# Kernel optimization log

Hardware: AMD Instinct MI355X
Metric: run time of the kernel (lower is better)

## Reference

```python
import jax, jax.numpy as jnp
import numpy as np

GROUP_SIZE = 64
M, K, N, RANK = 4096, 4096, 4096, 32


def setup_inputs() -> dict:
    key = jax.random.key(0)
    ks = jax.random.split(key, 7)
    x = jax.random.normal(ks[0], (M, K), dtype=jnp.float32)
    # int4 weight residual in [-8, 7]
    q_w = jax.random.randint(ks[1], (K, N), -8, 8, dtype=jnp.int32)
    # positive per-group weight scales, shape (K // group_size, N)
    wscales = jax.random.uniform(ks[2], (K // GROUP_SIZE, N), dtype=jnp.float32) * 0.01 + 1e-4
    lora_down = jax.random.normal(ks[3], (K, RANK), dtype=jnp.float32) * 0.02
    lora_up = jax.random.normal(ks[4], (RANK, N), dtype=jnp.float32) * 0.02
    # smoothing factors, strictly positive
    smooth = jax.random.uniform(ks[5], (K,), dtype=jnp.float32) + 0.5
    bias = jax.random.normal(ks[6], (N,), dtype=jnp.float32)
    return {"x": x, "q_w": q_w, "wscales": wscales, "lora_down": lora_down,
            "lora_up": lora_up, "smooth": smooth, "bias": bias}


def reference(x, q_w, wscales, lora_down, lora_up, smooth, bias):
    G = GROUP_SIZE
    m, k = x.shape
    n = q_w.shape[1]
    ng = k // G  # groups along K

    # smooth activation: move outliers into weights
    x_smooth = x / smooth[None, :]

    # per-group symmetric int4 quantize + dequantize of activations
    xg = x_smooth.reshape(m, ng, G)
    ascales = jnp.maximum(jnp.max(jnp.abs(xg), axis=-1) / 7.0, 1e-8)  # (m, ng)
    qx = jnp.clip(jnp.round(xg / ascales[..., None]), -8.0, 7.0)
    x_dq = (qx * ascales[..., None]).reshape(m, k)

    # dequantize int4 weight residual: grouped along K
    W_dq = (q_w.astype(jnp.float32).reshape(ng, G, n) * wscales[:, None, :]).reshape(k, n)

    # simulated int4 GEMM + fp LoRA residual + bias
    y_main = x_dq @ W_dq
    y_lora = (x @ lora_down) @ lora_up
    return y_main + y_lora + bias[None, :]
```

## Files before the change

kernel.cpp:

```cpp
#include <hip/hip_runtime.h>
#include <hip/hip_bf16.h>
#include <stdint.h>

#define GSIZE 64
#define MDIM 4096
#define KDIM 4096
#define NDIM 4096
#define RANK 32
#define KE   4160
#define NG   64
#define NSPLIT 8

#define N_LORATQ 256
#define N_WPREP  (65 * 64)
#define NBLOCKS  (N_LORATQ + N_WPREP)

typedef __bf16 bf16x4 __attribute__((ext_vector_type(4)));
typedef __bf16 bf16x8 __attribute__((ext_vector_type(8)));
typedef float  f32x4  __attribute__((ext_vector_type(4)));

#define GPTR(p) ((__attribute__((address_space(1))) void*)(uintptr_t)(p))
#define LPTR(p) ((__attribute__((address_space(3))) void*)(p))

__global__ __launch_bounds__(512) void k_prep(const float* __restrict__ x,
                                              const int*   __restrict__ qw,
                                              const float* __restrict__ wsc,
                                              const float* __restrict__ ld,
                                              const float* __restrict__ lu,
                                              const float* __restrict__ smooth,
                                              __bf16* __restrict__ A,
                                              __bf16* __restrict__ Wt,
                                              float* __restrict__ tws) {
    __shared__ __attribute__((aligned(16))) char smem[81920];
    int b   = blockIdx.x;
    int tid = threadIdx.x;

    if (b < N_LORATQ) {
        __bf16* Xs  = (__bf16*)smem;
        __bf16* BsL = (__bf16*)(smem + 65536);
        int m0 = (b & 31) * 128;
        int sp = b >> 5;
        int lane = tid & 63;
        int wave = tid >> 6;
        int quad = lane >> 4;
        int mrow = lane & 15;
        int c4   = tid & 63;

        f32x4 z = {0.f, 0.f, 0.f, 0.f};
        f32x4 acc[2];
        acc[0] = z; acc[1] = z;

        #pragma unroll
        for (int sub = 0; sub < 2; ++sub) {
            int kb = sp * 512 + sub * 256;

            #pragma unroll
            for (int i = 0; i < 16; ++i) {
                int idx = i * 512 + tid;
                int k = idx >> 5, n = idx & 31;
                *(__bf16*)((char*)BsL + n * 512 +
                           ((((k >> 3) ^ (n & 7)) << 4) | ((k & 7) << 1)))
                    = (__bf16)ld[(size_t)(kb + k) * RANK + n];
            }

            {
                float4 sv = *(const float4*)(smooth + kb + c4 * 4);
                float4 si = {__builtin_amdgcn_rcpf(sv.x), __builtin_amdgcn_rcpf(sv.y),
                             __builtin_amdgcn_rcpf(sv.z), __builtin_amdgcn_rcpf(sv.w)};
                int g = c4 >> 1;
                #pragma unroll 4
                for (int p = 0; p < 16; ++p) {
                    int row = wave + 8 * p;
                    float4 xv = *(const float4*)(x + (size_t)(m0 + row) * KDIM + kb + c4 * 4);
                    float4 xs = {xv.x * si.x, xv.y * si.y, xv.z * si.z, xv.w * si.w};
                    float a = fmaxf(fmaxf(fabsf(xs.x), fabsf(xs.y)),
                                    fmaxf(fabsf(xs.z), fabsf(xs.w)));
                    #pragma unroll
                    for (int off = 1; off < 16; off <<= 1)
                        a = fmaxf(a, __shfl_xor(a, off, 64));
                    float ascale = fmaxf(a * (1.0f / 7.0f), 1e-8f);
                    float rin = __builtin_amdgcn_rcpf(ascale);
                    float q0 = fminf(fmaxf(rintf(xs.x * rin), -8.f), 7.f);
                    float q1 = fminf(fmaxf(rintf(xs.y * rin), -8.f), 7.f);
                    float q2 = fminf(fmaxf(rintf(xs.z * rin), -8.f), 7.f);
                    float q3 = fminf(fmaxf(rintf(xs.w * rin), -8.f), 7.f);
                    bf16x4 aq = {(__bf16)(q0 * ascale), (__bf16)(q1 * ascale),
                                 (__bf16)(q2 * ascale), (__bf16)(q3 * ascale)};
                    *(bf16x4*)(A + (size_t)(m0 + row) * KE + kb + c4 * 4) = aq;
                    bf16x4 xb = {(__bf16)xv.x, (__bf16)xv.y, (__bf16)xv.z, (__bf16)xv.w};
                    *(bf16x4*)((char*)Xs + row * 512 +
                               (((g ^ (row & 7)) << 4) | ((c4 & 1) << 3))) = xb;
                }
            }
            __syncthreads();

            #pragma unroll
            for (int step = 0; step < 8; ++step) {
                int row = wave * 16 + mrow;
                bf16x8 av = *(const bf16x8*)((char*)Xs + row * 512 +
                                             (((step * 4 + quad) ^ (row & 7)) << 4));
                #pragma unroll
                for (int j = 0; j < 2; ++j) {
                    int n = j * 16 + mrow;
                    bf16x8 bv = *(const bf16x8*)((char*)BsL + n * 512 +
                                                 (((step * 4 + quad) ^ (n & 7)) << 4));
                    acc[j] = __builtin_amdgcn_mfma_f32_16x16x32_bf16(av, bv, acc[j], 0, 0, 0);
                }
            }
            __syncthreads();
        }

        float* tout = tws + (size_t)sp * MDIM * RANK;
        #pragma unroll
        for (int j = 0; j < 2; ++j)
            #pragma unroll
            for (int r = 0; r < 4; ++r) {
                int rowg = m0 + wave * 16 + quad * 4 + r;
                int col  = j * 16 + mrow;
                tout[(size_t)rowg * RANK + col] = acc[j][r];
            }
        return;
    }

    {
        __bf16 (*tile)[65] = (__bf16(*)[65])smem;
        int widx = b - N_LORATQ;
        int n0 = (widx & 63) * 64;
        int kt = widx >> 6;
        int k0 = kt * 64;
        int tr = tid >> 4;
        int tc = (tid & 15) * 4;
        if (kt < NG) {
            float4 ws = *(const float4*)(wsc + (size_t)kt * NDIM + n0 + tc);
            #pragma unroll
            for (int r = tr; r < 64; r += 32) {
                int4 q = *(const int4*)(qw + (size_t)(k0 + r) * NDIM + n0 + tc);
                tile[r][tc + 0] = (__bf16)((float)q.x * ws.x);
                tile[r][tc + 1] = (__bf16)((float)q.y * ws.y);
                tile[r][tc + 2] = (__bf16)((float)q.z * ws.z);
                tile[r][tc + 3] = (__bf16)((float)q.w * ws.w);
            }
        } else {
            #pragma unroll
            for (int r = tr; r < 64; r += 32) {
                if (r < RANK) {
                    float4 lv = *(const float4*)(lu + (size_t)r * NDIM + n0 + tc);
                    tile[r][tc + 0] = (__bf16)lv.x;
                    tile[r][tc + 1] = (__bf16)lv.y;
                    tile[r][tc + 2] = (__bf16)lv.z;
                    tile[r][tc + 3] = (__bf16)lv.w;
                } else {
                    tile[r][tc + 0] = (__bf16)0.f;
                    tile[r][tc + 1] = (__bf16)0.f;
                    tile[r][tc + 2] = (__bf16)0.f;
                    tile[r][tc + 3] = (__bf16)0.f;
                }
            }
        }
        __syncthreads();
        int nn = tid >> 3;
        int ks = (tid & 7) * 8;
        bf16x8 v;
        #pragma unroll
        for (int e = 0; e < 8; ++e) v[e] = tile[ks + e][nn];
        *(bf16x8*)(Wt + (size_t)(n0 + nn) * KE + k0 + ks) = v;
    }
}

__global__ __launch_bounds__(256) void k_fin(const float* __restrict__ tws,
                                             __bf16* __restrict__ A) {
    int idx = blockIdx.x * 256 + threadIdx.x;
    int m = idx >> 4, cq = idx & 15;
    int c = cq * 4;
    bf16x4 v = {(__bf16)0.f, (__bf16)0.f, (__bf16)0.f, (__bf16)0.f};
    if (c < RANK) {
        f32x4 s = {0.f, 0.f, 0.f, 0.f};
        #pragma unroll
        for (int sp = 0; sp < NSPLIT; ++sp) {
            f32x4 p = *(const f32x4*)(tws + ((size_t)sp * MDIM + m) * RANK + c);
            s.x += p.x; s.y += p.y; s.z += p.z; s.w += p.w;
        }
        v[0] = (__bf16)s.x; v[1] = (__bf16)s.y; v[2] = (__bf16)s.z; v[3] = (__bf16)s.w;
    }
    *(bf16x4*)(A + (size_t)m * KE + KDIM + c) = v;
}

#define NT (KE / 64)
#define HS 8192
#define BS 16384

#define STAGE(ldsbase, gb, kt, half) do {                                     \
    int _k0 = (kt) * 64;                                                      \
    _Pragma("unroll")                                                         \
    for (int _it = 0; _it < 2; ++_it) {                                       \
        int _c = _it * 512 + tid;                                             \
        int _r = _c >> 3;                                                     \
        int _g = (_c & 7) ^ (_r & 7);                                         \
        __builtin_amdgcn_global_load_lds(                                     \
            GPTR((gb) + (size_t)((half) * 128 + _r) * KE + _k0 + _g * 8),     \
            LPTR((char*)(ldsbase) + (_it * 512 + wave * 64) * 16),            \
            16, 0, 0);                                                        \
    } } while (0)

#define RD_A(dst, base, qm) do {                                              \
    _Pragma("unroll")                                                         \
    for (int _i = 0; _i < 4; ++_i) {                                          \
        int _row = (qm) * 128 + wm * 64 + _i * 16 + mrow;                     \
        dst[0][_i] = *(const bf16x8*)((const char*)(base) + _row * 128 + ga0 * 16); \
        dst[1][_i] = *(const bf16x8*)((const char*)(base) + _row * 128 + ga1 * 16); \
    } } while (0)

#define RD_B(dst, base, qn) do {                                              \
    _Pragma("unroll")                                                         \
    for (int _j = 0; _j < 2; ++_j) {                                          \
        int _row = (qn) * 128 + wn * 32 + _j * 16 + mrow;                     \
        dst[0][_j] = *(const bf16x8*)((const char*)(base) + _row * 128 + ga0 * 16); \
        dst[1][_j] = *(const bf16x8*)((const char*)(base) + _row * 128 + ga1 * 16); \
    } } while (0)

#define MMA(qm, qn, AV, BV) do {                                              \
    _Pragma("unroll")                                                         \
    for (int _i = 0; _i < 4; ++_i)                                            \
        _Pragma("unroll")                                                     \
        for (int _j = 0; _j < 2; ++_j) {                                      \
            acc[qm][qn][_i][_j] = __builtin_amdgcn_mfma_f32_16x16x32_bf16(    \
                AV[0][_i], BV[0][_j], acc[qm][qn][_i][_j], 0, 0, 0);          \
            acc[qm][qn][_i][_j] = __builtin_amdgcn_mfma_f32_16x16x32_bf16(    \
                AV[1][_i], BV[1][_j], acc[qm][qn][_i][_j], 0, 0, 0);          \
        } } while (0)

#define SBAR0() __builtin_amdgcn_sched_barrier(0)

__global__ __launch_bounds__(512, 2) void k_gemm(const __bf16* __restrict__ A,
                                                 const __bf16* __restrict__ Wt,
                                                 const float*  __restrict__ bias,
                                                 float* __restrict__ out) {
    __shared__ __attribute__((aligned(16))) __bf16 As[2 * BS];
    __shared__ __attribute__((aligned(16))) __bf16 Bs[2 * BS];
    int tid  = threadIdx.x;
    int lane = tid & 63;
    int wave = tid >> 6;
    int quad = lane >> 4;
    int mrow = lane & 15;
    int wm = wave >> 2;
    int wn = wave & 3;

    int lin = blockIdx.y * 16 + blockIdx.x;
    int swz = (lin & 7) * 32 + (lin >> 3);
    int m0 = (swz >> 4) * 256, n0 = (swz & 15) * 256;

    const __bf16* Ab = A  + (size_t)m0 * KE;
    const __bf16* Bb = Wt + (size_t)n0 * KE;

    int ga0 = quad ^ (mrow & 7);
    int ga1 = (quad + 4) ^ (mrow & 7);

    f32x4 z = {0.f, 0.f, 0.f, 0.f};
    f32x4 acc[2][2][4][2];
    #pragma unroll
    for (int a = 0; a < 2; ++a)
        #pragma unroll
        for (int b = 0; b < 2; ++b)
            #pragma unroll
            for (int i = 0; i < 4; ++i)
                #pragma unroll
                for (int j = 0; j < 2; ++j) acc[a][b][i][j] = z;

    STAGE(As,           Ab, 0, 0);
    STAGE(Bs + HS,      Bb, 0, 1);
    STAGE(Bs,           Bb, 0, 0);
    STAGE(As + HS,      Ab, 0, 1);
    STAGE(As + BS,      Ab, 1, 0);
    STAGE(Bs + BS + HS, Bb, 1, 1);
    asm volatile("s_waitcnt vmcnt(4)" ::: "memory");
    __builtin_amdgcn_s_barrier();
    SBAR0();

    bf16x8 av0[2][4], av1[2][4], bv0[2][2], bv1[2][2];
    RD_A(av0, As, 0);
    RD_B(bv0, Bs, 0);
    SBAR0();

    for (int t = 0; t < NT; ++t) {
        int cur = t & 1;
        const __bf16* Acur = As + cur * BS;
        const __bf16* Bcur = Bs + cur * BS;
        __bf16* Anx = As + (cur ^ 1) * BS;
        __bf16* Bnx = Bs + (cur ^ 1) * BS;
        __bf16* Acu = As + cur * BS;
        __bf16* Bcu = Bs + cur * BS;
        bool s1 = (t + 1 < NT), s2 = (t + 2 < NT);

        if (s1) STAGE(Bnx, Bb, t + 1, 0);
        RD_B(bv1, Bcur, 1);
        SBAR0();
        asm volatile("s_waitcnt lgkmcnt(4)" ::: "memory");
        SBAR0();
        __builtin_amdgcn_s_setprio(1);
        MMA(0, 0, av0, bv0);
        __builtin_amdgcn_s_setprio(0);

        if (s1) STAGE(Anx + HS, Ab, t + 1, 1);
        RD_A(av1, Acur, 1);
        SBAR0();
        asm volatile("s_waitcnt lgkmcnt(8)" ::: "memory");
        SBAR0();
        __builtin_amdgcn_s_setprio(1);
        MMA(0, 1, av0, bv1);
        __builtin_amdgcn_s_setprio(0);
        __builtin_amdgcn_s_barrier();
        SBAR0();

        if (s2) STAGE(Acu, Ab, t + 2, 0);
        SBAR0();
        asm volatile("s_waitcnt lgkmcnt(0)" ::: "memory");
        SBAR0();
        __builtin_amdgcn_s_setprio(1);
        MMA(1, 1, av1, bv1);
        __builtin_amdgcn_s_setprio(0);
        if (s2) { asm volatile("s_waitcnt vmcnt(2)" ::: "memory"); }
        else    { asm volatile("s_waitcnt vmcnt(0)" ::: "memory"); }
        __builtin_amdgcn_s_barrier();
        SBAR0();

        if (s2) STAGE(Bcu + HS, Bb, t + 2, 1);
        if (s1) RD_A(av0, Anx, 0);
        SBAR0();
        __builtin_amdgcn_s_setprio(1);
        MMA(1, 0, av1, bv0);
        __builtin_amdgcn_s_setprio(0);
        if (s1) RD_B(bv0, Bnx, 0);
        SBAR0();
    }

    #pragma unroll
    for (int qn = 0; qn < 2; ++qn)
        #pragma unroll
        for (int j = 0; j < 2; ++j) {
            int col = n0 + qn * 128 + wn * 32 + j * 16 + mrow;
            float bvs = bias[col];
            #pragma unroll
            for (int qm = 0; qm < 2; ++qm)
                #pragma unroll
                for (int i = 0; i < 4; ++i) {
                    int rbase = m0 + qm * 128 + wm * 64 + i * 16 + quad * 4;
                    #pragma unroll
                    for (int r = 0; r < 4; ++r)
                        __builtin_nontemporal_store(acc[qm][qn][i][j][r] + bvs,
                                                    &out[(size_t)(rbase + r) * NDIM + col]);
                }
        }
}

extern "C" void kernel_launch(void* const* d_in, const int* in_sizes, int n_in,
                              void* d_out, int out_size, void* d_ws, size_t ws_size,
                              hipStream_t stream) {
    const float* x    = (const float*)d_in[0];
    const int*   qw   = (const int*)  d_in[1];
    const float* wsc  = (const float*)d_in[2];
    const float* ld   = (const float*)d_in[3];
    const float* lu   = (const float*)d_in[4];
    const float* sm   = (const float*)d_in[5];
    const float* bias = (const float*)d_in[6];
    float* out = (float*)d_out;

    char* ws = (char*)d_ws;
    __bf16* A   = (__bf16*)ws;
    __bf16* Wt  = (__bf16*)(ws + (size_t)MDIM * KE * 2);
    float*  tws = (float*) (ws + (size_t)MDIM * KE * 4);

    k_prep<<<NBLOCKS, 512, 0, stream>>>(x, qw, wsc, ld, lu, sm, A, Wt, tws);
    k_fin<<<(MDIM * 16) / 256, 256, 0, stream>>>(tws, A);
    k_gemm<<<dim3(NDIM / 256, MDIM / 256), 512, 0, stream>>>(A, Wt, bias, out);
}
```

Measured before the change: 309.6 us.

## Fuse LoRA down-projection reduction into prep kernel and drop k_fin launch

The LoRA block split is reworked: each of the 256 blocks now owns 16 rows across the full K range instead of 128 rows over a K-split, and reduces its per-wave MFMA partials in shared memory before writing the bf16 rank columns straight into A. This removes the split-K fp32 workspace, the separate reduction kernel and one launch, and shrinks shared memory from 80KB to 24KB, which should allow more resident blocks. Weight int loads become nontemporal to avoid cache pollution. The trade-off is that each LoRA block runs a longer serial loop of 16 chunks with only one MFMA step per chunk and two barriers each.

```diff
diff --git a/kernel.cpp b/kernel.cpp
--- a/kernel.cpp
+++ b/kernel.cpp
@@ -9,7 +9,6 @@
 #define RANK 32
 #define KE   4160
 #define NG   64
-#define NSPLIT 8
 
 #define N_LORATQ 256
 #define N_WPREP  (65 * 64)
@@ -18,6 +17,7 @@
 typedef __bf16 bf16x4 __attribute__((ext_vector_type(4)));
 typedef __bf16 bf16x8 __attribute__((ext_vector_type(8)));
 typedef float  f32x4  __attribute__((ext_vector_type(4)));
+typedef long long llx2 __attribute__((ext_vector_type(2)));
 
 #define GPTR(p) ((__attribute__((address_space(1))) void*)(uintptr_t)(p))
 #define LPTR(p) ((__attribute__((address_space(3))) void*)(p))
@@ -29,37 +29,36 @@
                                               const float* __restrict__ lu,
                                               const float* __restrict__ smooth,
                                               __bf16* __restrict__ A,
-                                              __bf16* __restrict__ Wt,
-                                              float* __restrict__ tws) {
-    __shared__ __attribute__((aligned(16))) char smem[81920];
+                                              __bf16* __restrict__ Wt) {
+    __shared__ __attribute__((aligned(16))) char smem[24576];
     int b   = blockIdx.x;
     int tid = threadIdx.x;
 
     if (b < N_LORATQ) {
         __bf16* Xs  = (__bf16*)smem;
-        __bf16* BsL = (__bf16*)(smem + 65536);
-        int m0 = (b & 31) * 128;
-        int sp = b >> 5;
+        __bf16* BsL = (__bf16*)(smem + 8192);
+        int m0   = b * 16;
         int lane = tid & 63;
         int wave = tid >> 6;
         int quad = lane >> 4;
         int mrow = lane & 15;
         int c4   = tid & 63;
+        int r0   = tid >> 6;
 
         f32x4 z = {0.f, 0.f, 0.f, 0.f};
         f32x4 acc[2];
         acc[0] = z; acc[1] = z;
 
-        #pragma unroll
-        for (int sub = 0; sub < 2; ++sub) {
-            int kb = sp * 512 + sub * 256;
+        for (int ch = 0; ch < 16; ++ch) {
+            int kb = ch * 256;
 
             #pragma unroll
             for (int i = 0; i < 16; ++i) {
                 int idx = i * 512 + tid;
                 int k = idx >> 5, n = idx & 31;
-                *(__bf16*)((char*)BsL + n * 512 +
-                           ((((k >> 3) ^ (n & 7)) << 4) | ((k & 7) << 1)))
+                int kg = k >> 3;
+                int sl = (kg & ~7) | ((kg & 7) ^ (n & 7));
+                *(__bf16*)((char*)BsL + n * 512 + (sl << 4) + (k & 7) * 2)
                     = (__bf16)ld[(size_t)(kb + k) * RANK + n];
             }
 
@@ -67,10 +66,10 @@
                 float4 sv = *(const float4*)(smooth + kb + c4 * 4);
                 float4 si = {__builtin_amdgcn_rcpf(sv.x), __builtin_amdgcn_rcpf(sv.y),
                              __builtin_amdgcn_rcpf(sv.z), __builtin_amdgcn_rcpf(sv.w)};
-                int g = c4 >> 1;
-                #pragma unroll 4
-                for (int p = 0; p < 16; ++p) {
-                    int row = wave + 8 * p;
+                int g = c4 >> 1, h = c4 & 1;
+                #pragma unroll
+                for (int p = 0; p < 2; ++p) {
+                    int row = r0 + p * 8;
                     float4 xv = *(const float4*)(x + (size_t)(m0 + row) * KDIM + kb + c4 * 4);
                     float4 xs = {xv.x * si.x, xv.y * si.y, xv.z * si.z, xv.w * si.w};
                     float a = fmaxf(fmaxf(fabsf(xs.x), fabsf(xs.y)),
@@ -87,38 +86,43 @@
                     bf16x4 aq = {(__bf16)(q0 * ascale), (__bf16)(q1 * ascale),
                                  (__bf16)(q2 * ascale), (__bf16)(q3 * ascale)};
                     *(bf16x4*)(A + (size_t)(m0 + row) * KE + kb + c4 * 4) = aq;
+                    int sl = (g & ~7) | ((g & 7) ^ (row & 7));
                     bf16x4 xb = {(__bf16)xv.x, (__bf16)xv.y, (__bf16)xv.z, (__bf16)xv.w};
-                    *(bf16x4*)((char*)Xs + row * 512 +
-                               (((g ^ (row & 7)) << 4) | ((c4 & 1) << 3))) = xb;
+                    *(bf16x4*)((char*)Xs + row * 512 + (sl << 4) + h * 8) = xb;
                 }
             }
             __syncthreads();
 
-            #pragma unroll
-            for (int step = 0; step < 8; ++step) {
-                int row = wave * 16 + mrow;
-                bf16x8 av = *(const bf16x8*)((char*)Xs + row * 512 +
-                                             (((step * 4 + quad) ^ (row & 7)) << 4));
+            {
+                int kg = wave * 4 + quad;
+                int sla = (kg & ~7) | ((kg & 7) ^ (mrow & 7));
+                bf16x8 av = *(const bf16x8*)((char*)Xs + mrow * 512 + (sla << 4));
                 #pragma unroll
                 for (int j = 0; j < 2; ++j) {
                     int n = j * 16 + mrow;
-                    bf16x8 bv = *(const bf16x8*)((char*)BsL + n * 512 +
-                                                 (((step * 4 + quad) ^ (n & 7)) << 4));
+                    int slb = (kg & ~7) | ((kg & 7) ^ (n & 7));
+                    bf16x8 bv = *(const bf16x8*)((char*)BsL + n * 512 + (slb << 4));
                     acc[j] = __builtin_amdgcn_mfma_f32_16x16x32_bf16(av, bv, acc[j], 0, 0, 0);
                 }
             }
             __syncthreads();
         }
 
-        float* tout = tws + (size_t)sp * MDIM * RANK;
+        float* scratch = (float*)smem;
         #pragma unroll
         for (int j = 0; j < 2; ++j)
             #pragma unroll
-            for (int r = 0; r < 4; ++r) {
-                int rowg = m0 + wave * 16 + quad * 4 + r;
-                int col  = j * 16 + mrow;
-                tout[(size_t)rowg * RANK + col] = acc[j][r];
-            }
+            for (int r = 0; r < 4; ++r)
+                scratch[wave * 512 + (quad * 4 + r) * 32 + j * 16 + mrow] = acc[j][r];
+        __syncthreads();
+        {
+            int m = tid >> 5, n = tid & 31;
+            float s = 0.f;
+            #pragma unroll
+            for (int w = 0; w < 8; ++w) s += scratch[w * 512 + m * 32 + n];
+            A[(size_t)(m0 + m) * KE + KDIM + n]      = (__bf16)s;
+            A[(size_t)(m0 + m) * KE + KDIM + 32 + n] = (__bf16)0.f;
+        }
         return;
     }
 
@@ -134,7 +138,9 @@
             float4 ws = *(const float4*)(wsc + (size_t)kt * NDIM + n0 + tc);
             #pragma unroll
             for (int r = tr; r < 64; r += 32) {
-                int4 q = *(const int4*)(qw + (size_t)(k0 + r) * NDIM + n0 + tc);
+                llx2 qraw = __builtin_nontemporal_load(
+                    (const llx2*)(qw + (size_t)(k0 + r) * NDIM + n0 + tc));
+                int4 q = *(const int4*)&qraw;
                 tile[r][tc + 0] = (__bf16)((float)q.x * ws.x);
                 tile[r][tc + 1] = (__bf16)((float)q.y * ws.y);
                 tile[r][tc + 2] = (__bf16)((float)q.z * ws.z);
@@ -167,24 +173,6 @@
     }
 }
 
-__global__ __launch_bounds__(256) void k_fin(const float* __restrict__ tws,
-                                             __bf16* __restrict__ A) {
-    int idx = blockIdx.x * 256 + threadIdx.x;
-    int m = idx >> 4, cq = idx & 15;
-    int c = cq * 4;
-    bf16x4 v = {(__bf16)0.f, (__bf16)0.f, (__bf16)0.f, (__bf16)0.f};
-    if (c < RANK) {
-        f32x4 s = {0.f, 0.f, 0.f, 0.f};
-        #pragma unroll
-        for (int sp = 0; sp < NSPLIT; ++sp) {
-            f32x4 p = *(const f32x4*)(tws + ((size_t)sp * MDIM + m) * RANK + c);
-            s.x += p.x; s.y += p.y; s.z += p.z; s.w += p.w;
-        }
-        v[0] = (__bf16)s.x; v[1] = (__bf16)s.y; v[2] = (__bf16)s.z; v[3] = (__bf16)s.w;
-    }
-    *(bf16x4*)(A + (size_t)m * KE + KDIM + c) = v;
-}
-
 #define NT (KE / 64)
 #define HS 8192
 #define BS 16384
@@ -367,9 +355,7 @@
     char* ws = (char*)d_ws;
     __bf16* A   = (__bf16*)ws;
     __bf16* Wt  = (__bf16*)(ws + (size_t)MDIM * KE * 2);
-    float*  tws = (float*) (ws + (size_t)MDIM * KE * 4);
-
-    k_prep<<<NBLOCKS, 512, 0, stream>>>(x, qw, wsc, ld, lu, sm, A, Wt, tws);
-    k_fin<<<(MDIM * 16) / 256, 256, 0, stream>>>(tws, A);
+
+    k_prep<<<NBLOCKS, 512, 0, stream>>>(x, qw, wsc, ld, lu, sm, A, Wt);
     k_gemm<<<dim3(NDIM / 256, MDIM / 256), 512, 0, stream>>>(A, Wt, bias, out);
 }
```

After: 389.4 us. 1.26x slower.
